# Optimization experiments

Hardware: AMD Instinct MI355X
Metric: run time of the kernel (lower is better)

The kernel has to match this reference:

```python
import jax, jax.numpy as jnp
import numpy as np

B, T, D = 32, 4096, 256
LN_EPS = 1e-5


def setup_inputs() -> dict:
    key = jax.random.key(0)
    k0, k1, k2 = jax.random.split(key, 3)
    byte_ids = jax.random.randint(k0, (B, T), 0, 256, dtype=jnp.int32)
    freq_bands = jnp.ones((D // 2,), jnp.float32)  # nn.Parameter(torch.ones(embed_dim//2))
    # freq_proj: Linear(D, 2D) -> LayerNorm(2D) -> GELU -> Linear(2D, D)
    w1 = jax.random.normal(k1, (D, 2 * D), jnp.float32) * (1.0 / np.sqrt(D))
    b1 = jnp.zeros((2 * D,), jnp.float32)
    gamma = jnp.ones((2 * D,), jnp.float32)
    beta = jnp.zeros((2 * D,), jnp.float32)
    w2 = jax.random.normal(k2, (2 * D, D), jnp.float32) * (1.0 / np.sqrt(2 * D))
    b2 = jnp.zeros((D,), jnp.float32)
    return dict(byte_ids=byte_ids, freq_bands=freq_bands, w1=w1, b1=b1,
                gamma=gamma, beta=beta, w2=w2, b2=b2)


def reference(byte_ids, freq_bands, w1, b1, gamma, beta, w2, b2):
    Bsz, Tlen = byte_ids.shape
    Dm = w1.shape[0]
    k = min(Dm // 2, Tlen // 2)  # static
    signal = byte_ids.astype(jnp.float32) / 127.5 - 1.0  # [B,T]
    # Single FFT; FFT(roll(signal, -pos))[f] == X[f] * exp(+2i*pi*f*pos/T),
    # so |spectrum| is position-invariant and angle shifts linearly in pos.
    X = jnp.fft.fft(signal, axis=1)[:, :k]           # [B,k] complex64
    mag = jnp.abs(X) * freq_bands[:k]                 # [B,k]
    phase0 = jnp.angle(X)                             # [B,k]
    pos = jnp.arange(Tlen, dtype=jnp.float32)
    f = jnp.arange(k, dtype=jnp.float32)
    shift = (2.0 * np.pi / Tlen) * pos[:, None] * f[None, :]      # [T,k]
    phase = phase0[:, None, :] + shift[None, :, :]                 # [B,T,k]
    mag_bt = jnp.broadcast_to(mag[:, None, :], (Bsz, Tlen, k))     # [B,T,k]
    feats = jnp.concatenate([mag_bt, jnp.sin(phase), jnp.cos(phase)], axis=-1)  # [B,T,3k]
    if feats.shape[-1] < Dm:
        feats = jnp.pad(feats, ((0, 0), (0, 0), (0, Dm - feats.shape[-1])))
    else:
        feats = feats[..., :Dm]                        # truncate (drops cos tail)
    # freq_proj MLP
    h = feats @ w1 + b1                                # [B,T,2D]
    mu = jnp.mean(h, axis=-1, keepdims=True)
    var = jnp.var(h, axis=-1, keepdims=True)
    h = (h - mu) * jax.lax.rsqrt(var + LN_EPS) * gamma + beta
    h = jax.nn.gelu(h, approximate=False)              # torch nn.GELU default = exact erf
    return h @ w2 + b2                                 # [B,T,D]
```

## Files before the change

kernel.cpp:

```cpp
#include <hip/hip_runtime.h>


#define T_SZ   4096
#define NFREQ  128

typedef short    bf16x8 __attribute__((ext_vector_type(8)));
typedef unsigned u32x4  __attribute__((ext_vector_type(4)));
typedef float    f32x4  __attribute__((ext_vector_type(4)));

__device__ __forceinline__ float bf2f(unsigned short x) {
  union { unsigned u; float f; } v; v.u = ((unsigned)x) << 16; return v.f;
}
__device__ __forceinline__ float bits2f(unsigned u) {
  union { unsigned u; float f; } v; v.u = u; return v.f;
}
__device__ __forceinline__ unsigned short f2bf(float x) {
  union { float f; unsigned u; } v; v.f = x;
  unsigned r = v.u + 0x7fffu + ((v.u >> 16) & 1u);
  return (unsigned short)(r >> 16);
}
__device__ __forceinline__ unsigned pk2(float lo, float hi) {
  union { float f; unsigned u; } a, b;
  a.f = lo; b.f = hi;
  return __builtin_amdgcn_perm(b.u + 0x8000u, a.u + 0x8000u, 0x07060302u);
}
__device__ __forceinline__ bf16x8 as_bf(u32x4 v) { return __builtin_bit_cast(bf16x8, v); }
__device__ __forceinline__ bool probe_f32(const unsigned* p) {
  return p[0] == 0x3F800000u;
}
__device__ __forceinline__ void stage16(const void* g, const void* lds_base) {
  __builtin_amdgcn_global_load_lds(
      (const __attribute__((address_space(1))) unsigned int*)g,
      (__attribute__((address_space(3))) unsigned int*)lds_base, 16, 0, 0);
}
__device__ __forceinline__ float gelu_f(float v) {
  float u = v * (0.7978845608f + 0.0356774081f * v * v);
  float d = 1.0f + exp2f(-2.885390082f * u);
  return v * __builtin_amdgcn_rcpf(d);
}

__global__ void dft_kernel(const int* __restrict__ ids,
                           const void* __restrict__ fb,
                           unsigned short* __restrict__ mag,
                           float* __restrict__ ph0) {
  bool f32 = probe_f32((const unsigned*)fb);
  int b  = blockIdx.x >> 3;
  int fg = blockIdx.x & 7;
  int fl = threadIdx.x >> 4;
  int m  = threadIdx.x & 15;
  int f  = fg * 16 + fl;
  const int* row = ids + b * T_SZ;
  const float C = 6.283185307179586f / 4096.0f;
  float re = 0.f, im = 0.f;
  for (int i = 0; i < 256; ++i) {
    int t = m + i * 16;
    float s = (float)row[t] * (1.0f / 127.5f) - 1.0f;
    float ang = (float)((t * f) & 4095) * C;
    re += s * __cosf(ang);
    im -= s * __sinf(ang);
  }
  #pragma unroll
  for (int mask = 1; mask < 16; mask <<= 1) {
    re += __shfl_xor(re, mask, 64);
    im += __shfl_xor(im, mask, 64);
  }
  if (m == 0) {
    float fbv = f32 ? ((const float*)fb)[f] : bf2f(((const unsigned short*)fb)[f]);
    float mg = sqrtf(re * re + im * im) * fbv;
    mag[b * NFREQ + f] = f2bf(mg);
    ph0[b * NFREQ + f] = atan2f(im, re);
  }
}

__global__ void prep_kernel(const void* __restrict__ w1, const void* __restrict__ w2,
                            const void* __restrict__ b1, const void* __restrict__ gamma,
                            const void* __restrict__ beta, const void* __restrict__ b2,
                            const unsigned* __restrict__ probe,
                            const unsigned short* __restrict__ mag,
                            unsigned short* __restrict__ w1sin,
                            unsigned short* __restrict__ w2tp,
                            unsigned short* __restrict__ bia,
                            float* __restrict__ hmag) {
  bool f32 = probe_f32(probe);
  int bid = blockIdx.x, tid = threadIdx.x;
  if (bid < 256) {
    int o = bid * 256 + tid;
    int f = o & 127, n1 = o >> 7;
    int idx = (128 + f) * 512 + n1;
    w1sin[o] = f32 ? f2bf(((const float*)w1)[idx]) : ((const unsigned short*)w1)[idx];
  } else if (bid < 768) {
    int o = (bid - 256) * 256 + tid;
    int p = o & 511, n2 = o >> 9;
    int n1 = ((p >> 5) << 5) | (((p >> 2) & 1) << 4) | (((p >> 3) & 3) << 2) | (p & 3);
    int idx = n1 * 256 + n2;
    w2tp[o] = f32 ? f2bf(((const float*)w2)[idx]) : ((const unsigned short*)w2)[idx];
  } else if (bid < 832) {
    int idx = (bid - 768) * 256 + tid;
    int n1 = idx & 511, b = idx >> 9;
    const unsigned short* mrow = mag + b * NFREQ;
    float acc = 0.f;
    for (int f = 0; f < 128; ++f) {
      float wv = f32 ? ((const float*)w1)[f * 512 + n1]
                     : bf2f(((const unsigned short*)w1)[f * 512 + n1]);
      acc += bf2f(mrow[f]) * bf2f(f2bf(wv));
    }
    float bv = f32 ? ((const float*)b1)[n1] : bf2f(((const unsigned short*)b1)[n1]);
    hmag[idx] = acc + bv;
  } else {
    int i = (bid - 832) * 256 + tid;
    const void* src; int off;
    if (i < 512)       { src = gamma; off = i; }
    else if (i < 1024) { src = beta;  off = i - 512; }
    else               { src = b2;    off = i - 1024; }
    bia[i] = f32 ? f2bf(((const float*)src)[off]) : ((const unsigned short*)src)[off];
  }
}

__global__ __launch_bounds__(256, 2)
void fused_kernel(const unsigned short* __restrict__ w1sin,
                  const unsigned short* __restrict__ w2tp,
                  const unsigned short* __restrict__ bias,
                  const float* __restrict__ hmag,
                  const float* __restrict__ ph0,
                  float* __restrict__ out) {
  __shared__ __align__(16) short lds_w[16384];

  const int tid  = threadIdx.x;
  const int wave = tid >> 6;
  const int lane = tid & 63;
  const int quad = lane >> 4;
  const int col  = lane & 15;

  const int blk  = blockIdx.x;
  const int b    = blk >> 5;
  const int my_t = ((blk & 31) << 6) + (wave << 4) + col;

  u32x4 BsA[4], BsB[4];
  const float* php = ph0 + b * NFREQ;
  const float PHC = 6.283185307179586f / 4096.0f;
  #pragma unroll
  for (int s = 0; s < 4; ++s) {
    u32x4 awA, awB;
    #pragma unroll
    for (int w = 0; w < 4; ++w) {
      int f0 = s * 32 + quad * 8 + w * 2;
      float a0 = __sinf(php[f0]     + (float)((my_t * f0) & 4095) * PHC);
      float a1 = __sinf(php[f0 + 1] + (float)((my_t * (f0 + 1)) & 4095) * PHC);
      awA[w] = pk2(a0, a1);
      awB[w] = awA[w] ^ 0x80000000u;
    }
    BsA[s] = awA; BsB[s] = awB;
  }

  const float* hmagb = hmag + b * 512;
  u32x4 B2A[16], B2B[16];
  float sumA = 0.f, ssqA = 0.f, sumB = 0.f, ssqB = 0.f;
  #pragma unroll
  for (int c = 0; c < 4; ++c) {
    #pragma unroll
    for (int i = 0; i < 8; ++i) {
      int rl = wave * 32 + i * 4 + (lane >> 4);
      int gchunk = (lane & 15) ^ (rl & 15);
      stage16(w1sin + ((c * 128 + rl) * 128 + gchunk * 8),
              lds_w + (wave * 32 + i * 4) * 128);
    }
    __syncthreads();
    f32x4 pA = {0.f, 0.f, 0.f, 0.f}, pB = {0.f, 0.f, 0.f, 0.f};
    #pragma unroll
    for (int ntl = 0; ntl < 8; ++ntl) {
      f32x4 aA = *(const f32x4*)(hmagb + c * 128 + ntl * 16 + 4 * quad);
      f32x4 aB = aA;
      #pragma unroll
      for (int s = 0; s < 4; ++s) {
        bf16x8 frag = *(const bf16x8*)(lds_w + (ntl * 16 + col) * 128
                                             + (((s * 4 + quad) ^ col) << 3));
        aA = __builtin_amdgcn_mfma_f32_16x16x32_bf16(frag, as_bf(BsA[s]), aA, 0, 0, 0);
        aB = __builtin_amdgcn_mfma_f32_16x16x32_bf16(frag, as_bf(BsB[s]), aB, 0, 0, 0);
      }
      #pragma unroll
      for (int jj = 0; jj < 4; ++jj) {
        sumA += aA[jj]; ssqA += aA[jj] * aA[jj];
        sumB += aB[jj]; ssqB += aB[jj] * aB[jj];
      }
      if ((ntl & 1) == 0) { pA = aA; pB = aB; }
      else {
        int s2l = ntl >> 1;
        u32x4 hA, hB;
        hA[0] = pk2(pA[0], pA[1]); hA[1] = pk2(pA[2], pA[3]);
        hA[2] = pk2(aA[0], aA[1]); hA[3] = pk2(aA[2], aA[3]);
        hB[0] = pk2(pB[0], pB[1]); hB[1] = pk2(pB[2], pB[3]);
        hB[2] = pk2(aB[0], aB[1]); hB[3] = pk2(aB[2], aB[3]);
        B2A[c * 4 + s2l] = hA;
        B2B[c * 4 + s2l] = hB;
      }
    }
    __syncthreads();
  }

  #pragma unroll
  for (int i = 0; i < 8; ++i) {
    int rl = i * 4 + wave;
    int gchunk = lane ^ (rl & 15);
    stage16(w2tp + (rl * 512 + gchunk * 8), lds_w + rl * 512);
  }

  sumA += __shfl_xor(sumA, 16, 64); sumA += __shfl_xor(sumA, 32, 64);
  ssqA += __shfl_xor(ssqA, 16, 64); ssqA += __shfl_xor(ssqA, 32, 64);
  sumB += __shfl_xor(sumB, 16, 64); sumB += __shfl_xor(sumB, 32, 64);
  ssqB += __shfl_xor(ssqB, 16, 64); ssqB += __shfl_xor(ssqB, 32, 64);
  float muA = sumA * (1.0f / 512.0f);
  float varA = fmaxf(ssqA * (1.0f / 512.0f) - muA * muA, 0.0f);
  float rsA = rsqrtf(varA + 1e-5f);
  float muB = sumB * (1.0f / 512.0f);
  float varB = fmaxf(ssqB * (1.0f / 512.0f) - muB * muB, 0.0f);
  float rsB = rsqrtf(varB + 1e-5f);

  const unsigned short* gptr  = bias;
  const unsigned short* beptr = bias + 512;
  #pragma unroll
  for (int s2 = 0; s2 < 16; ++s2) {
    u32x4 hwA = B2A[s2], hwB = B2B[s2], owA, owB;
    #pragma unroll
    for (int w = 0; w < 4; ++w) {
      int nt  = 2 * s2 + (w >> 1);
      int n1b = nt * 16 + 4 * quad + (w & 1) * 2;
      unsigned gp = *(const unsigned*)(gptr + n1b);
      unsigned bp = *(const unsigned*)(beptr + n1b);
      float g0 = bits2f(gp << 16),  g1 = bits2f(gp & 0xffff0000u);
      float e0 = bits2f(bp << 16),  e1 = bits2f(bp & 0xffff0000u);
      float hA0 = bits2f(hwA[w] << 16), hA1 = bits2f(hwA[w] & 0xffff0000u);
      float hB0 = bits2f(hwB[w] << 16), hB1 = bits2f(hwB[w] & 0xffff0000u);
      float tA0 = rsA * g0, tA1 = rsA * g1;
      float tB0 = rsB * g0, tB1 = rsB * g1;
      float vA0 = fmaf(hA0, tA0, fmaf(-muA, tA0, e0));
      float vA1 = fmaf(hA1, tA1, fmaf(-muA, tA1, e1));
      float vB0 = fmaf(hB0, tB0, fmaf(-muB, tB0, e0));
      float vB1 = fmaf(hB1, tB1, fmaf(-muB, tB1, e1));
      owA[w] = pk2(gelu_f(vA0), gelu_f(vA1));
      owB[w] = pk2(gelu_f(vB0), gelu_f(vB1));
    }
    B2A[s2] = owA;
    B2B[s2] = owB;
  }

  const unsigned short* b2p = bias + 1024;
  const long orowA = (long)(b * T_SZ + my_t) * 256;
  const long orowB = orowA + (long)2048 * 256;
  #pragma unroll
  for (int c2 = 0; c2 < 8; ++c2) {
    __syncthreads();
    #pragma unroll
    for (int n2l = 0; n2l < 2; ++n2l) {
      int n2t = c2 * 2 + n2l;
      f32x4 ccA = {0.f, 0.f, 0.f, 0.f};
      f32x4 ccB = {0.f, 0.f, 0.f, 0.f};
      #pragma unroll
      for (int s2 = 0; s2 < 16; ++s2) {
        bf16x8 A2 = *(const bf16x8*)(lds_w + (n2l * 16 + col) * 512
                                           + (((s2 * 4 + quad) ^ col) << 3));
        ccA = __builtin_amdgcn_mfma_f32_16x16x32_bf16(A2, as_bf(B2A[s2]), ccA, 0, 0, 0);
        ccB = __builtin_amdgcn_mfma_f32_16x16x32_bf16(A2, as_bf(B2B[s2]), ccB, 0, 0, 0);
      }
      unsigned bp0 = *(const unsigned*)(b2p + n2t * 16 + 4 * quad);
      unsigned bp1 = *(const unsigned*)(b2p + n2t * 16 + 4 * quad + 2);
      float bb0 = bits2f(bp0 << 16), bb1 = bits2f(bp0 & 0xffff0000u);
      float bb2 = bits2f(bp1 << 16), bb3 = bits2f(bp1 & 0xffff0000u);
      ccA[0] += bb0; ccA[1] += bb1; ccA[2] += bb2; ccA[3] += bb3;
      ccB[0] += bb0; ccB[1] += bb1; ccB[2] += bb2; ccB[3] += bb3;
      *(f32x4*)(out + orowA + n2t * 16 + quad * 4) = ccA;
      *(f32x4*)(out + orowB + n2t * 16 + quad * 4) = ccB;
    }
    __syncthreads();
    if (c2 < 7) {
      #pragma unroll
      for (int i = 0; i < 8; ++i) {
        int rl = i * 4 + wave;
        int gchunk = lane ^ (rl & 15);
        stage16(w2tp + (((c2 + 1) * 32 + rl) * 512 + gchunk * 8), lds_w + rl * 512);
      }
    }
  }
}

extern "C" void kernel_launch(void* const* d_in, const int* in_sizes, int n_in,
                              void* d_out, int out_size, void* d_ws, size_t ws_size,
                              hipStream_t stream) {
  const int*      ids   = (const int*)d_in[0];
  const void*     fb    = d_in[1];
  const void*     w1    = d_in[2];
  const void*     b1    = d_in[3];
  const void*     gamma = d_in[4];
  const void*     beta  = d_in[5];
  const void*     w2    = d_in[6];
  const void*     b2    = d_in[7];
  float*          out   = (float*)d_out;
  const unsigned* probe = (const unsigned*)fb;

  char* ws = (char*)d_ws;
  unsigned short* mag   = (unsigned short*)(ws);
  float*          ph0   = (float*)(ws + 8192);
  unsigned short* bia   = (unsigned short*)(ws + 24576);
  float*          hmag  = (float*)(ws + 32768);
  unsigned short* w1sin = (unsigned short*)(ws + 98304);
  unsigned short* w2tp  = (unsigned short*)(ws + 229376);

  dft_kernel<<<dim3(32 * 8), dim3(256), 0, stream>>>(ids, fb, mag, ph0);
  prep_kernel<<<dim3(837), dim3(256), 0, stream>>>(w1, w2, b1, gamma, beta, b2,
                                                   probe, mag, w1sin, w2tp, bia, hmag);
  fused_kernel<<<dim3(1024), dim3(256), 0, stream>>>(w1sin, w2tp, bia, hmag, ph0, out);
}
```

Measured before the change: 265.4 us.

## Double-buffer LDS weight staging to overlap loads with MFMA compute

Splits the shared weight buffer into two halves and prefetches the next W1/W2 chunk into one half while MFMAs consume the other. Chunk sizes are halved (64 rows of W1, 16 rows of W2) so both buffers fit in the existing LDS allocation. The first W2 chunk is prefetched during the final W1 step. This replaces the serial stage-sync-compute-sync pattern with one barrier per step, hiding global-to-LDS latency. The trade-off is twice as many, smaller stages and iterations.

```diff
diff --git a/kernel.cpp b/kernel.cpp
--- a/kernel.cpp
+++ b/kernel.cpp
@@ -135,6 +135,16 @@
   const int b    = blk >> 5;
   const int my_t = ((blk & 31) << 6) + (wave << 4) + col;
 
+  {
+    short* bufp = lds_w;
+    #pragma unroll
+    for (int i = 0; i < 4; ++i) {
+      int rl = wave * 16 + i * 4 + quad;
+      int gch = (lane & 15) ^ (rl & 15);
+      stage16(w1sin + ((0 * 64 + rl) * 128 + gch * 8), bufp + (wave * 16 + i * 4) * 128);
+    }
+  }
+
   u32x4 BsA[4], BsB[4];
   const float* php = ph0 + b * NFREQ;
   const float PHC = 6.283185307179586f / 4096.0f;
@@ -152,28 +162,40 @@
     BsA[s] = awA; BsB[s] = awB;
   }
 
+  __syncthreads();
+
   const float* hmagb = hmag + b * 512;
   u32x4 B2A[16], B2B[16];
   float sumA = 0.f, ssqA = 0.f, sumB = 0.f, ssqB = 0.f;
   #pragma unroll
-  for (int c = 0; c < 4; ++c) {
-    #pragma unroll
-    for (int i = 0; i < 8; ++i) {
-      int rl = wave * 32 + i * 4 + (lane >> 4);
-      int gchunk = (lane & 15) ^ (rl & 15);
-      stage16(w1sin + ((c * 128 + rl) * 128 + gchunk * 8),
-              lds_w + (wave * 32 + i * 4) * 128);
-    }
-    __syncthreads();
+  for (int h = 0; h < 8; ++h) {
+    short* cur = lds_w + (h & 1) * 8192;
+    short* nxt = lds_w + ((h + 1) & 1) * 8192;
+    if (h < 7) {
+      #pragma unroll
+      for (int i = 0; i < 4; ++i) {
+        int rl = wave * 16 + i * 4 + quad;
+        int gch = (lane & 15) ^ (rl & 15);
+        stage16(w1sin + (((h + 1) * 64 + rl) * 128 + gch * 8),
+                nxt + (wave * 16 + i * 4) * 128);
+      }
+    } else {
+      #pragma unroll
+      for (int i = 0; i < 4; ++i) {
+        int rl = i * 4 + wave;
+        int gch = lane ^ (rl & 15);
+        stage16(w2tp + ((0 * 16 + rl) * 512 + gch * 8), nxt + rl * 512);
+      }
+    }
     f32x4 pA = {0.f, 0.f, 0.f, 0.f}, pB = {0.f, 0.f, 0.f, 0.f};
     #pragma unroll
-    for (int ntl = 0; ntl < 8; ++ntl) {
-      f32x4 aA = *(const f32x4*)(hmagb + c * 128 + ntl * 16 + 4 * quad);
+    for (int ntl = 0; ntl < 4; ++ntl) {
+      f32x4 aA = *(const f32x4*)(hmagb + h * 64 + ntl * 16 + 4 * quad);
       f32x4 aB = aA;
       #pragma unroll
       for (int s = 0; s < 4; ++s) {
-        bf16x8 frag = *(const bf16x8*)(lds_w + (ntl * 16 + col) * 128
-                                             + (((s * 4 + quad) ^ col) << 3));
+        bf16x8 frag = *(const bf16x8*)(cur + (ntl * 16 + col) * 128
+                                           + (((s * 4 + quad) ^ col) << 3));
         aA = __builtin_amdgcn_mfma_f32_16x16x32_bf16(frag, as_bf(BsA[s]), aA, 0, 0, 0);
         aB = __builtin_amdgcn_mfma_f32_16x16x32_bf16(frag, as_bf(BsB[s]), aB, 0, 0, 0);
       }
@@ -184,24 +206,17 @@
       }
       if ((ntl & 1) == 0) { pA = aA; pB = aB; }
       else {
-        int s2l = ntl >> 1;
+        int s2l = h * 2 + (ntl >> 1);
         u32x4 hA, hB;
         hA[0] = pk2(pA[0], pA[1]); hA[1] = pk2(pA[2], pA[3]);
         hA[2] = pk2(aA[0], aA[1]); hA[3] = pk2(aA[2], aA[3]);
         hB[0] = pk2(pB[0], pB[1]); hB[1] = pk2(pB[2], pB[3]);
         hB[2] = pk2(aB[0], aB[1]); hB[3] = pk2(aB[2], aB[3]);
-        B2A[c * 4 + s2l] = hA;
-        B2B[c * 4 + s2l] = hB;
+        B2A[s2l] = hA;
+        B2B[s2l] = hB;
       }
     }
     __syncthreads();
-  }
-
-  #pragma unroll
-  for (int i = 0; i < 8; ++i) {
-    int rl = i * 4 + wave;
-    int gchunk = lane ^ (rl & 15);
-    stage16(w2tp + (rl * 512 + gchunk * 8), lds_w + rl * 512);
   }
 
   sumA += __shfl_xor(sumA, 16, 64); sumA += __shfl_xor(sumA, 32, 64);
@@ -247,38 +262,34 @@
   const long orowA = (long)(b * T_SZ + my_t) * 256;
   const long orowB = orowA + (long)2048 * 256;
   #pragma unroll
-  for (int c2 = 0; c2 < 8; ++c2) {
-    __syncthreads();
-    #pragma unroll
-    for (int n2l = 0; n2l < 2; ++n2l) {
-      int n2t = c2 * 2 + n2l;
-      f32x4 ccA = {0.f, 0.f, 0.f, 0.f};
-      f32x4 ccB = {0.f, 0.f, 0.f, 0.f};
-      #pragma unroll
-      for (int s2 = 0; s2 < 16; ++s2) {
-        bf16x8 A2 = *(const bf16x8*)(lds_w + (n2l * 16 + col) * 512
-                                           + (((s2 * 4 + quad) ^ col) << 3));
-        ccA = __builtin_amdgcn_mfma_f32_16x16x32_bf16(A2, as_bf(B2A[s2]), ccA, 0, 0, 0);
-        ccB = __builtin_amdgcn_mfma_f32_16x16x32_bf16(A2, as_bf(B2B[s2]), ccB, 0, 0, 0);
-      }
-      unsigned bp0 = *(const unsigned*)(b2p + n2t * 16 + 4 * quad);
-      unsigned bp1 = *(const unsigned*)(b2p + n2t * 16 + 4 * quad + 2);
-      float bb0 = bits2f(bp0 << 16), bb1 = bits2f(bp0 & 0xffff0000u);
-      float bb2 = bits2f(bp1 << 16), bb3 = bits2f(bp1 & 0xffff0000u);
-      ccA[0] += bb0; ccA[1] += bb1; ccA[2] += bb2; ccA[3] += bb3;
-      ccB[0] += bb0; ccB[1] += bb1; ccB[2] += bb2; ccB[3] += bb3;
-      *(f32x4*)(out + orowA + n2t * 16 + quad * 4) = ccA;
-      *(f32x4*)(out + orowB + n2t * 16 + quad * 4) = ccB;
-    }
-    __syncthreads();
-    if (c2 < 7) {
-      #pragma unroll
-      for (int i = 0; i < 8; ++i) {
+  for (int h = 0; h < 16; ++h) {
+    short* cur = lds_w + (h & 1) * 8192;
+    short* nxt = lds_w + ((h + 1) & 1) * 8192;
+    if (h < 15) {
+      #pragma unroll
+      for (int i = 0; i < 4; ++i) {
         int rl = i * 4 + wave;
-        int gchunk = lane ^ (rl & 15);
-        stage16(w2tp + (((c2 + 1) * 32 + rl) * 512 + gchunk * 8), lds_w + rl * 512);
-      }
-    }
+        int gch = lane ^ (rl & 15);
+        stage16(w2tp + (((h + 1) * 16 + rl) * 512 + gch * 8), nxt + rl * 512);
+      }
+    }
+    f32x4 ccA = {0.f, 0.f, 0.f, 0.f};
+    f32x4 ccB = {0.f, 0.f, 0.f, 0.f};
+    #pragma unroll
+    for (int s2 = 0; s2 < 16; ++s2) {
+      bf16x8 A2 = *(const bf16x8*)(cur + col * 512 + (((s2 * 4 + quad) ^ col) << 3));
+      ccA = __builtin_amdgcn_mfma_f32_16x16x32_bf16(A2, as_bf(B2A[s2]), ccA, 0, 0, 0);
+      ccB = __builtin_amdgcn_mfma_f32_16x16x32_bf16(A2, as_bf(B2B[s2]), ccB, 0, 0, 0);
+    }
+    unsigned bp0 = *(const unsigned*)(b2p + h * 16 + 4 * quad);
+    unsigned bp1 = *(const unsigned*)(b2p + h * 16 + 4 * quad + 2);
+    float bb0 = bits2f(bp0 << 16), bb1 = bits2f(bp0 & 0xffff0000u);
+    float bb2 = bits2f(bp1 << 16), bb3 = bits2f(bp1 & 0xffff0000u);
+    ccA[0] += bb0; ccA[1] += bb1; ccA[2] += bb2; ccA[3] += bb3;
+    ccB[0] += bb0; ccB[1] += bb1; ccB[2] += bb2; ccB[3] += bb3;
+    *(f32x4*)(out + orowA + h * 16 + quad * 4) = ccA;
+    *(f32x4*)(out + orowB + h * 16 + quad * 4) = ccB;
+    if (h < 15) __syncthreads();
   }
 }
 
```

Result: faster. 258.9 us (-2.4%).
